# Kernel optimization log

Measured on AMD Instinct MI355X. Metric: run time of the kernel, lower is better.

## Reference

```python
import jax, jax.numpy as jnp
import numpy as np

T, K, D_SLOTS, D_IN, D_HID, EPSILON = 3, 11, 64, 128, 256, 1e-8


def _layer_norm(x, g, b, eps=1e-5):
    m = jnp.mean(x, axis=-1, keepdims=True)
    v = jnp.mean((x - m) ** 2, axis=-1, keepdims=True)
    return (x - m) * jax.lax.rsqrt(v + eps) * g + b


def _gru_cell(x, h, w_ih, w_hh, b_ih, b_hh):
    # torch.nn.GRUCell math; w_ih/w_hh stored as [D, 3D] (input-major)
    gx = x @ w_ih + b_ih
    gh = h @ w_hh + b_hh
    xr, xz, xn = jnp.split(gx, 3, axis=-1)
    hr, hz, hn = jnp.split(gh, 3, axis=-1)
    r = jax.nn.sigmoid(xr + hr)
    z = jax.nn.sigmoid(xz + hz)
    n = jnp.tanh(xn + r * hn)
    return (1.0 - z) * n + z * h


def setup_inputs() -> dict:
    key = jax.random.key(0)
    ks = jax.random.split(key, 12)
    B, N = 64, 4096
    s = 0.02
    return {
        "inputs": jax.random.normal(ks[0], (B, N, D_IN), jnp.float32),
        "ln_in_g": jnp.ones((D_IN,), jnp.float32),
        "ln_in_b": jnp.zeros((D_IN,), jnp.float32),
        "Wk": jax.random.normal(ks[1], (D_IN, D_SLOTS), jnp.float32) * s,
        "Wv": jax.random.normal(ks[2], (D_IN, D_SLOTS), jnp.float32) * s,
        "init_latents": jax.random.normal(ks[3], (1, K, D_SLOTS), jnp.float32),
        "ln_q_g": jnp.ones((D_SLOTS,), jnp.float32),
        "ln_q_b": jnp.zeros((D_SLOTS,), jnp.float32),
        "Wq": jax.random.normal(ks[4], (D_SLOTS, D_SLOTS), jnp.float32) * s,
        "w_ih": jax.random.normal(ks[5], (D_SLOTS, 3 * D_SLOTS), jnp.float32) * s,
        "w_hh": jax.random.normal(ks[6], (D_SLOTS, 3 * D_SLOTS), jnp.float32) * s,
        "b_ih": jnp.zeros((3 * D_SLOTS,), jnp.float32),
        "b_hh": jnp.zeros((3 * D_SLOTS,), jnp.float32),
        "ln_f_g": jnp.ones((D_SLOTS,), jnp.float32),
        "ln_f_b": jnp.zeros((D_SLOTS,), jnp.float32),
        "W1": jax.random.normal(ks[7], (D_SLOTS, D_HID), jnp.float32) * s,
        "b1": jnp.zeros((D_HID,), jnp.float32),
        "W2": jax.random.normal(ks[8], (D_HID, D_SLOTS), jnp.float32) * s,
        "b2": jnp.zeros((D_SLOTS,), jnp.float32),
    }


def reference(inputs, ln_in_g, ln_in_b, Wk, Wv, init_latents, ln_q_g, ln_q_b, Wq,
              w_ih, w_hh, b_ih, b_hh, ln_f_g, ln_f_b, W1, b1, W2, b2):
    B = inputs.shape[0]
    x = _layer_norm(inputs, ln_in_g, ln_in_b)          # [B,N,128]
    keys = x @ Wk                                       # [B,N,D]
    vals = x @ Wv                                       # [B,N,D]
    slots = jnp.broadcast_to(init_latents, (B, K, D_SLOTS))
    scale = D_SLOTS ** (-0.5)
    attn2 = None
    for _ in range(T):
        slots_prev = slots
        q = _layer_norm(slots, ln_q_g, ln_q_b) @ Wq     # [B,K,D]
        logits = scale * jnp.einsum('bnc,bmc->bnm', keys, q)  # [B,N,K]
        attn = jax.nn.softmax(logits, axis=-1) + EPSILON
        attn2 = attn
        attn_n = attn / jnp.sum(attn, axis=1, keepdims=True)   # competing norm over inputs
        updates = jnp.einsum('bnm,bnc->bmc', attn_n, vals)     # [B,K,D]
        slots = _gru_cell(updates.reshape(B * K, D_SLOTS),
                          slots_prev.reshape(B * K, D_SLOTS),
                          w_ih, w_hh, b_ih, b_hh).reshape(B, K, D_SLOTS)
        h = jax.nn.relu(_layer_norm(slots, ln_f_g, ln_f_b) @ W1 + b1)
        slots = slots + (h @ W2 + b2)
    return slots, attn2
```

## Files before the change

### kernel.cpp

```cpp
#include <hip/hip_runtime.h>

#define DIN   128
#define DSL   64
#define KSL   11
#define NTOK  4096
#define NB    64
#define NSPLIT 32
#define LN_EPS   1e-5f
#define ATTN_EPS 1e-8f
#define SCALE    0.125f

typedef __bf16 bf16x8 __attribute__((ext_vector_type(8)));
typedef float  f32x4  __attribute__((ext_vector_type(4)));

__global__ void k_prep(const float* __restrict__ Wk, const float* __restrict__ Wv,
                       const float* __restrict__ g, const float* __restrict__ b,
                       __bf16* __restrict__ WTf, float* __restrict__ EP) {
  if (blockIdx.x == 8) {
    const int c = threadIdx.x;
    if (c < 128) {
      const float* __restrict__ W = (c < 64) ? Wk : Wv;
      const int cc = c & 63;
      float G = 0.f, Bt = 0.f;
      for (int k = 0; k < 128; ++k) {
        const float w = W[k * 64 + cc];
        G += g[k] * w; Bt += b[k] * w;
      }
      EP[c] = G; EP[128 + c] = Bt;
    }
    return;
  }
  const int t = blockIdx.x * 256 + threadIdx.x;
  const int fid = t >> 6, lane = t & 63;
  const int ks = fid >> 3, nt = fid & 7;
  const int col = nt * 16 + (lane & 15);
  const int kb  = ks * 32 + (lane >> 4) * 8;
  union { uint4 u; __bf16 h[8]; } o;
#pragma unroll
  for (int j = 0; j < 8; ++j) {
    const int k = kb + j;
    const float v = ((col < 64) ? Wk[k * 64 + col] : Wv[k * 64 + (col - 64)]) * g[k];
    o.h[j] = (__bf16)v;
  }
  *((uint4*)WTf + t) = o.u;
}

__launch_bounds__(256)
__global__ void k_lnproj(const float* __restrict__ inp, const __bf16* __restrict__ WTf,
                         const float* __restrict__ EP, __bf16* __restrict__ keys,
                         __bf16* __restrict__ valsT) {
  __shared__ __bf16 Xs[4][16][136];
  __shared__ float rowstats[4][16][2];
  const int tid = threadIdx.x, wave = tid >> 6, lane = tid & 63;
  const int half = lane >> 5, hl = lane & 31;
  const int t = lane & 15, g = lane >> 4;
  const int rbase = blockIdx.x * 64 + wave * 16;

  float4 xr[8];
#pragma unroll
  for (int p = 0; p < 8; ++p)
    xr[p] = *(const float4*)(inp + (size_t)(rbase + 2 * p + half) * DIN + hl * 4);

  float s[8], sq[8];
#pragma unroll
  for (int p = 0; p < 8; ++p) {
    s[p]  = xr[p].x + xr[p].y + xr[p].z + xr[p].w;
    sq[p] = xr[p].x * xr[p].x + xr[p].y * xr[p].y + xr[p].z * xr[p].z + xr[p].w * xr[p].w;
    union { ushort4 u; __bf16 h[4]; } pk;
    pk.h[0] = (__bf16)xr[p].x; pk.h[1] = (__bf16)xr[p].y;
    pk.h[2] = (__bf16)xr[p].z; pk.h[3] = (__bf16)xr[p].w;
    *(ushort4*)&Xs[wave][2 * p + half][hl * 4] = pk.u;
  }

#pragma unroll
  for (int o = 16; o > 0; o >>= 1) {
#pragma unroll
    for (int p = 0; p < 8; ++p) { s[p] += __shfl_xor(s[p], o); sq[p] += __shfl_xor(sq[p], o); }
  }
  if (hl < 8) {
    const int p = hl;
    const float m = s[p] * (1.f / 128.f);
    const float rstd = rsqrtf(sq[p] * (1.f / 128.f) - m * m + LN_EPS);
    rowstats[wave][2 * p + half][0] = m;
    rowstats[wave][2 * p + half][1] = rstd;
  }

  const bf16x8* __restrict__ Wv8 = (const bf16x8*)WTf;
  bf16x8 wf[8];
#pragma unroll
  for (int nt = 0; nt < 8; ++nt) wf[nt] = Wv8[nt * 64 + lane];
  f32x4 acc[8] = {};
#pragma unroll
  for (int ks = 0; ks < 4; ++ks) {
    const bf16x8 xf = *(const bf16x8*)&Xs[wave][t][ks * 32 + g * 8];
    bf16x8 wn[8];
    if (ks < 3) {
#pragma unroll
      for (int nt = 0; nt < 8; ++nt) wn[nt] = Wv8[((ks + 1) * 8 + nt) * 64 + lane];
    }
#pragma unroll
    for (int nt = 0; nt < 8; ++nt)
      acc[nt] = __builtin_amdgcn_mfma_f32_16x16x32_bf16(wf[nt], xf, acc[nt], 0, 0, 0);
#pragma unroll
    for (int nt = 0; nt < 8; ++nt) wf[nt] = wn[nt];
  }

  const float2 mrs = *(const float2*)&rowstats[wave][t][0];
  const float rstd = mrs.y, mm = mrs.x * mrs.y;
  const int bidx = rbase >> 12;
  const int tIB  = (rbase & 4095) + t;
#pragma unroll
  for (int nt = 0; nt < 8; ++nt) {
    const float4 Gv = *(const float4*)(EP + nt * 16 + g * 4);
    const float4 Bv = *(const float4*)(EP + 128 + nt * 16 + g * 4);
    float o0 = rstd * acc[nt][0] - mm * Gv.x + Bv.x;
    float o1 = rstd * acc[nt][1] - mm * Gv.y + Bv.y;
    float o2 = rstd * acc[nt][2] - mm * Gv.z + Bv.z;
    float o3 = rstd * acc[nt][3] - mm * Gv.w + Bv.w;
    if (nt < 4) {
      union { unsigned long long u; __bf16 h[4]; } pk;
      pk.h[0] = (__bf16)o0; pk.h[1] = (__bf16)o1; pk.h[2] = (__bf16)o2; pk.h[3] = (__bf16)o3;
      *(unsigned long long*)&keys[(size_t)(rbase + t) * 64 + nt * 16 + g * 4] = pk.u;
    } else {
      const int vc = (nt - 4) * 16 + g * 4;
      valsT[((size_t)bidx * 64 + vc + 0) * NTOK + tIB] = (__bf16)o0;
      valsT[((size_t)bidx * 64 + vc + 1) * NTOK + tIB] = (__bf16)o1;
      valsT[((size_t)bidx * 64 + vc + 2) * NTOK + tIB] = (__bf16)o2;
      valsT[((size_t)bidx * 64 + vc + 3) * NTOK + tIB] = (__bf16)o3;
    }
  }
}

__global__ void k_init(const float* __restrict__ init_lat, const float* __restrict__ qg,
                       const float* __restrict__ qb, const float* __restrict__ Wq,
                       float* __restrict__ slots, float* __restrict__ q) {
  const int b = blockIdx.x;
  const int k = threadIdx.x >> 6, c = threadIdx.x & 63;
  const float s = init_lat[k * DSL + c];
  slots[(size_t)(b * KSL + k) * DSL + c] = s;
  float sum = s, sq = s * s;
#pragma unroll
  for (int o = 32; o > 0; o >>= 1) { sum += __shfl_xor(sum, o); sq += __shfl_xor(sq, o); }
  const float m = sum * (1.f / 64.f);
  const float rstd = rsqrtf(sq * (1.f / 64.f) - m * m + LN_EPS);
  const float qn = (s - m) * rstd * qg[c] + qb[c];
  float acc = 0.f;
  for (int i = 0; i < DSL; ++i) acc += __shfl(qn, i) * Wq[i * DSL + c];
  q[(size_t)(b * KSL + k) * DSL + c] = acc * SCALE;
}

__launch_bounds__(64)
__global__ void k_attn(const __bf16* __restrict__ keys, const __bf16* __restrict__ valsT,
                       const float* __restrict__ q, float* __restrict__ Upart,
                       float* __restrict__ Spart, float* __restrict__ attn_out) {
  __shared__ __bf16 P[2][16][72];
  const int b = blockIdx.x >> 5, sp = blockIdx.x & 31;
  const int lane = threadIdx.x;
  const int g = lane >> 4, t = lane & 15;

  bf16x8 qf[2];
#pragma unroll
  for (int ks = 0; ks < 2; ++ks) {
    float4 q0 = {0.f, 0.f, 0.f, 0.f}, q1 = {0.f, 0.f, 0.f, 0.f};
    if (t < KSL) {
      const float* __restrict__ qp = q + (size_t)(b * KSL + t) * DSL + ks * 32 + g * 8;
      q0 = *(const float4*)qp; q1 = *(const float4*)(qp + 4);
    }
    qf[ks][0] = (__bf16)q0.x; qf[ks][1] = (__bf16)q0.y;
    qf[ks][2] = (__bf16)q0.z; qf[ks][3] = (__bf16)q0.w;
    qf[ks][4] = (__bf16)q1.x; qf[ks][5] = (__bf16)q1.y;
    qf[ks][6] = (__bf16)q1.z; qf[ks][7] = (__bf16)q1.w;
  }

  const __bf16* __restrict__ kbase = keys + ((size_t)b * NTOK + sp * 128) * DSL;
  float sacc[4] = {0.f, 0.f, 0.f, 0.f};
  f32x4 U[4] = {};

#pragma unroll
  for (int gr = 0; gr < 2; ++gr) {
    const int tb = gr * 64;
#pragma unroll
    for (int tile = 0; tile < 4; ++tile) {
      f32x4 c = {};
#pragma unroll
      for (int ks = 0; ks < 2; ++ks) {
        const bf16x8 kf = *(const bf16x8*)(kbase + (size_t)(tb + tile * 16 + t) * DSL
                                           + ks * 32 + g * 8);
        c = __builtin_amdgcn_mfma_f32_16x16x32_bf16(qf[ks], kf, c, 0, 0, 0);
      }
      float lg[4];
#pragma unroll
      for (int r = 0; r < 4; ++r)
        lg[r] = (4 * g + r < KSL) ? c[r] : -1e30f;
      float mx = fmaxf(fmaxf(lg[0], lg[1]), fmaxf(lg[2], lg[3]));
      mx = fmaxf(mx, __shfl_xor(mx, 16));
      mx = fmaxf(mx, __shfl_xor(mx, 32));
      float e[4];
#pragma unroll
      for (int r = 0; r < 4; ++r) e[r] = __expf(lg[r] - mx);
      float se = e[0] + e[1] + e[2] + e[3];
      se += __shfl_xor(se, 16);
      se += __shfl_xor(se, 32);
      const float inv = 1.f / se;
#pragma unroll
      for (int r = 0; r < 4; ++r) {
        const float a = e[r] * inv + ATTN_EPS;
        sacc[r] += a;
        P[gr][4 * g + r][tile * 16 + t] = (__bf16)a;
        if (attn_out && 4 * g + r < KSL)
          attn_out[((size_t)b * NTOK + sp * 128 + tb + tile * 16 + t) * KSL + 4 * g + r] = a;
      }
    }
#pragma unroll
    for (int ks = 0; ks < 2; ++ks) {
      const bf16x8 pf = *(const bf16x8*)&P[gr][t][ks * 32 + g * 8];
#pragma unroll
      for (int ct = 0; ct < 4; ++ct) {
        const bf16x8 vf = *(const bf16x8*)(valsT + ((size_t)b * DSL + ct * 16 + t) * NTOK
                                           + sp * 128 + tb + ks * 32 + g * 8);
        U[ct] = __builtin_amdgcn_mfma_f32_16x16x32_bf16(pf, vf, U[ct], 0, 0, 0);
      }
    }
  }

  float* __restrict__ up = Upart + (size_t)(b * NSPLIT + sp) * (KSL * DSL);
#pragma unroll
  for (int ct = 0; ct < 4; ++ct)
#pragma unroll
    for (int r = 0; r < 4; ++r)
      if (4 * g + r < KSL) up[(4 * g + r) * DSL + ct * 16 + t] = U[ct][r];

#pragma unroll
  for (int r = 0; r < 4; ++r) {
#pragma unroll
    for (int o = 1; o < 16; o <<= 1) sacc[r] += __shfl_xor(sacc[r], o);
  }
  if (t == 0) {
    float* __restrict__ spp = Spart + (size_t)(b * NSPLIT + sp) * 16;
#pragma unroll
    for (int r = 0; r < 4; ++r) spp[4 * g + r] = sacc[r];
  }
}

__launch_bounds__(64)
__global__ void k_update(const float* __restrict__ Upart, const float* __restrict__ Spart,
                         float* __restrict__ slots, const float* __restrict__ w_ih,
                         const float* __restrict__ w_hh, const float* __restrict__ b_ih,
                         const float* __restrict__ b_hh, const float* __restrict__ fg,
                         const float* __restrict__ fb, const float* __restrict__ W1,
                         const float* __restrict__ b1v, const float* __restrict__ W2,
                         const float* __restrict__ b2v, const float* __restrict__ qg,
                         const float* __restrict__ qbv, const float* __restrict__ Wq,
                         float* __restrict__ q, float* __restrict__ out_slots) {
  const int row = blockIdx.x;
  const int c = threadIdx.x;
  const int b = row / 11, k = row - b * 11;

  float u = 0.f;
  for (int s = 0; s < NSPLIT; ++s)
    u += Upart[((size_t)(b * NSPLIT + s) * KSL + k) * DSL + c];
  float ss = 0.f;
  for (int s = 0; s < NSPLIT; ++s)
    ss += Spart[(size_t)(b * NSPLIT + s) * 16 + k];
  u /= ss;

  const float h = slots[(size_t)row * DSL + c];

  float gr = b_ih[c], gz = b_ih[64 + c], gn = b_ih[128 + c];
  float hr = b_hh[c], hz = b_hh[64 + c], hn = b_hh[128 + c];
  for (int i = 0; i < 64; ++i) {
    const float ui = __shfl(u, i), hi = __shfl(h, i);
    gr += ui * w_ih[i * 192 + c];       hr += hi * w_hh[i * 192 + c];
    gz += ui * w_ih[i * 192 + 64 + c];  hz += hi * w_hh[i * 192 + 64 + c];
    gn += ui * w_ih[i * 192 + 128 + c]; hn += hi * w_hh[i * 192 + 128 + c];
  }
  const float r = 1.f / (1.f + __expf(-(gr + hr)));
  const float z = 1.f / (1.f + __expf(-(gz + hz)));
  const float nn = tanhf(gn + r * hn);
  float sv = (1.f - z) * nn + z * h;

  float sum = sv, sq = sv * sv;
#pragma unroll
  for (int o = 32; o > 0; o >>= 1) { sum += __shfl_xor(sum, o); sq += __shfl_xor(sq, o); }
  float m = sum * (1.f / 64.f);
  float rstd = rsqrtf(sq * (1.f / 64.f) - m * m + LN_EPS);
  const float sl = (sv - m) * rstd * fg[c] + fb[c];

  float h0 = b1v[c], h1 = b1v[64 + c], h2 = b1v[128 + c], h3 = b1v[192 + c];
  for (int i = 0; i < 64; ++i) {
    const float si = __shfl(sl, i);
    h0 += si * W1[i * 256 + c];        h1 += si * W1[i * 256 + 64 + c];
    h2 += si * W1[i * 256 + 128 + c];  h3 += si * W1[i * 256 + 192 + c];
  }
  h0 = fmaxf(h0, 0.f); h1 = fmaxf(h1, 0.f); h2 = fmaxf(h2, 0.f); h3 = fmaxf(h3, 0.f);

  float o = b2v[c];
  for (int j = 0; j < 64; ++j) o += __shfl(h0, j) * W2[j * DSL + c];
  for (int j = 0; j < 64; ++j) o += __shfl(h1, j) * W2[(64 + j) * DSL + c];
  for (int j = 0; j < 64; ++j) o += __shfl(h2, j) * W2[(128 + j) * DSL + c];
  for (int j = 0; j < 64; ++j) o += __shfl(h3, j) * W2[(192 + j) * DSL + c];
  sv += o;

  slots[(size_t)row * DSL + c] = sv;
  if (out_slots) out_slots[(size_t)row * DSL + c] = sv;

  float s2 = sv, q2 = sv * sv;
#pragma unroll
  for (int o2 = 32; o2 > 0; o2 >>= 1) { s2 += __shfl_xor(s2, o2); q2 += __shfl_xor(q2, o2); }
  m = s2 * (1.f / 64.f);
  rstd = rsqrtf(q2 * (1.f / 64.f) - m * m + LN_EPS);
  const float qn = (sv - m) * rstd * qg[c] + qbv[c];
  float qa = 0.f;
  for (int i = 0; i < 64; ++i) qa += __shfl(qn, i) * Wq[i * DSL + c];
  q[(size_t)row * DSL + c] = qa * SCALE;
}

extern "C" void kernel_launch(void* const* d_in, const int* in_sizes, int n_in,
                              void* d_out, int out_size, void* d_ws, size_t ws_size,
                              hipStream_t stream) {
  const float* inp  = (const float*)d_in[0];
  const float* lng  = (const float*)d_in[1];
  const float* lnb  = (const float*)d_in[2];
  const float* Wk   = (const float*)d_in[3];
  const float* Wv   = (const float*)d_in[4];
  const float* init = (const float*)d_in[5];
  const float* qg   = (const float*)d_in[6];
  const float* qbb  = (const float*)d_in[7];
  const float* Wq   = (const float*)d_in[8];
  const float* wih  = (const float*)d_in[9];
  const float* whh  = (const float*)d_in[10];
  const float* bih  = (const float*)d_in[11];
  const float* bhh  = (const float*)d_in[12];
  const float* fg   = (const float*)d_in[13];
  const float* fb   = (const float*)d_in[14];
  const float* W1   = (const float*)d_in[15];
  const float* b1   = (const float*)d_in[16];
  const float* W2   = (const float*)d_in[17];
  const float* b2   = (const float*)d_in[18];

  char* wsb = (char*)d_ws;
  __bf16* keys  = (__bf16*)wsb;
  __bf16* valsT = keys + (size_t)NB * NTOK * DSL;
  __bf16* WTf   = valsT + (size_t)NB * DSL * NTOK;
  float* EP    = (float*)(WTf + 16384);
  float* slots = EP + 256;
  float* q     = slots + NB * KSL * DSL;
  float* Upart = q + NB * KSL * DSL;
  float* Spart = Upart + (size_t)NB * NSPLIT * KSL * DSL;

  float* out_slots = (float*)d_out;
  float* out_attn  = (float*)d_out + NB * KSL * DSL;

  k_prep<<<9, 256, 0, stream>>>(Wk, Wv, lng, lnb, WTf, EP);
  k_lnproj<<<4096, 256, 0, stream>>>(inp, WTf, EP, keys, valsT);
  k_init<<<NB, KSL * 64, 0, stream>>>(init, qg, qbb, Wq, slots, q);
  for (int t = 0; t < 3; ++t) {
    k_attn<<<NB * NSPLIT, 64, 0, stream>>>(keys, valsT, q, Upart, Spart,
                                           t == 2 ? out_attn : nullptr);
    k_update<<<NB * KSL, 64, 0, stream>>>(Upart, Spart, slots, wih, whh, bih, bhh,
                                          fg, fb, W1, b1, W2, b2, qg, qbb, Wq, q,
                                          t == 2 ? out_slots : nullptr);
  }
}
```

Baseline: 185.2 us.

## Split LN/projection into stats and proj kernels with LDS-transposed value stores

Splits the fused layernorm+projection kernel into a stats kernel that writes bf16 inputs and per-row mean/rstd to global memory, and a projection kernel that processes 32 tokens per wave with MFMA. The value outputs are staged through shared memory and written as coalesced 16-byte rows, replacing the scattered 2-byte transposed stores. The cost is an extra global round trip of the bf16 input copy plus an additional kernel launch.

```diff
diff --git a/kernel.cpp b/kernel.cpp
--- a/kernel.cpp
+++ b/kernel.cpp
@@ -46,14 +46,10 @@
 }
 
 __launch_bounds__(256)
-__global__ void k_lnproj(const float* __restrict__ inp, const __bf16* __restrict__ WTf,
-                         const float* __restrict__ EP, __bf16* __restrict__ keys,
-                         __bf16* __restrict__ valsT) {
-  __shared__ __bf16 Xs[4][16][136];
-  __shared__ float rowstats[4][16][2];
+__global__ void k_stats(const float* __restrict__ inp, __bf16* __restrict__ xbf,
+                        float2* __restrict__ stats) {
   const int tid = threadIdx.x, wave = tid >> 6, lane = tid & 63;
   const int half = lane >> 5, hl = lane & 31;
-  const int t = lane & 15, g = lane >> 4;
   const int rbase = blockIdx.x * 64 + wave * 16;
 
   float4 xr[8];
@@ -69,9 +65,8 @@
     union { ushort4 u; __bf16 h[4]; } pk;
     pk.h[0] = (__bf16)xr[p].x; pk.h[1] = (__bf16)xr[p].y;
     pk.h[2] = (__bf16)xr[p].z; pk.h[3] = (__bf16)xr[p].w;
-    *(ushort4*)&Xs[wave][2 * p + half][hl * 4] = pk.u;
-  }
-
+    *(ushort4*)&xbf[(size_t)(rbase + 2 * p + half) * DIN + hl * 4] = pk.u;
+  }
 #pragma unroll
   for (int o = 16; o > 0; o >>= 1) {
 #pragma unroll
@@ -81,54 +76,66 @@
     const int p = hl;
     const float m = s[p] * (1.f / 128.f);
     const float rstd = rsqrtf(sq[p] * (1.f / 128.f) - m * m + LN_EPS);
-    rowstats[wave][2 * p + half][0] = m;
-    rowstats[wave][2 * p + half][1] = rstd;
-  }
-
+    stats[rbase + 2 * p + half] = make_float2(m, rstd);
+  }
+}
+
+__launch_bounds__(256)
+__global__ void k_proj(const __bf16* __restrict__ xbf, const float2* __restrict__ stats,
+                       const __bf16* __restrict__ WTf, const float* __restrict__ EP,
+                       __bf16* __restrict__ keys, __bf16* __restrict__ valsT) {
+  __shared__ __bf16 VT[64][130];
+  const int tid = threadIdx.x, wave = tid >> 6, lane = tid & 63;
+  const int t = lane & 15, g = lane >> 4;
+  const int blkTok = blockIdx.x * 128;
+  const int tokbase = blkTok + wave * 32;
   const bf16x8* __restrict__ Wv8 = (const bf16x8*)WTf;
-  bf16x8 wf[8];
-#pragma unroll
-  for (int nt = 0; nt < 8; ++nt) wf[nt] = Wv8[nt * 64 + lane];
-  f32x4 acc[8] = {};
+
+  f32x4 acc[2][8] = {};
 #pragma unroll
   for (int ks = 0; ks < 4; ++ks) {
-    const bf16x8 xf = *(const bf16x8*)&Xs[wave][t][ks * 32 + g * 8];
-    bf16x8 wn[8];
-    if (ks < 3) {
-#pragma unroll
-      for (int nt = 0; nt < 8; ++nt) wn[nt] = Wv8[((ks + 1) * 8 + nt) * 64 + lane];
-    }
-#pragma unroll
-    for (int nt = 0; nt < 8; ++nt)
-      acc[nt] = __builtin_amdgcn_mfma_f32_16x16x32_bf16(wf[nt], xf, acc[nt], 0, 0, 0);
-#pragma unroll
-    for (int nt = 0; nt < 8; ++nt) wf[nt] = wn[nt];
-  }
-
-  const float2 mrs = *(const float2*)&rowstats[wave][t][0];
-  const float rstd = mrs.y, mm = mrs.x * mrs.y;
-  const int bidx = rbase >> 12;
-  const int tIB  = (rbase & 4095) + t;
-#pragma unroll
-  for (int nt = 0; nt < 8; ++nt) {
-    const float4 Gv = *(const float4*)(EP + nt * 16 + g * 4);
-    const float4 Bv = *(const float4*)(EP + 128 + nt * 16 + g * 4);
-    float o0 = rstd * acc[nt][0] - mm * Gv.x + Bv.x;
-    float o1 = rstd * acc[nt][1] - mm * Gv.y + Bv.y;
-    float o2 = rstd * acc[nt][2] - mm * Gv.z + Bv.z;
-    float o3 = rstd * acc[nt][3] - mm * Gv.w + Bv.w;
-    if (nt < 4) {
-      union { unsigned long long u; __bf16 h[4]; } pk;
-      pk.h[0] = (__bf16)o0; pk.h[1] = (__bf16)o1; pk.h[2] = (__bf16)o2; pk.h[3] = (__bf16)o3;
-      *(unsigned long long*)&keys[(size_t)(rbase + t) * 64 + nt * 16 + g * 4] = pk.u;
-    } else {
-      const int vc = (nt - 4) * 16 + g * 4;
-      valsT[((size_t)bidx * 64 + vc + 0) * NTOK + tIB] = (__bf16)o0;
-      valsT[((size_t)bidx * 64 + vc + 1) * NTOK + tIB] = (__bf16)o1;
-      valsT[((size_t)bidx * 64 + vc + 2) * NTOK + tIB] = (__bf16)o2;
-      valsT[((size_t)bidx * 64 + vc + 3) * NTOK + tIB] = (__bf16)o3;
-    }
-  }
+    const bf16x8 xf0 = *(const bf16x8*)&xbf[(size_t)(tokbase + t) * DIN + ks * 32 + g * 8];
+    const bf16x8 xf1 = *(const bf16x8*)&xbf[(size_t)(tokbase + 16 + t) * DIN + ks * 32 + g * 8];
+#pragma unroll
+    for (int nt = 0; nt < 8; ++nt) {
+      const bf16x8 wf = Wv8[(ks * 8 + nt) * 64 + lane];
+      acc[0][nt] = __builtin_amdgcn_mfma_f32_16x16x32_bf16(wf, xf0, acc[0][nt], 0, 0, 0);
+      acc[1][nt] = __builtin_amdgcn_mfma_f32_16x16x32_bf16(wf, xf1, acc[1][nt], 0, 0, 0);
+    }
+  }
+#pragma unroll
+  for (int tt = 0; tt < 2; ++tt) {
+    const float2 st = stats[tokbase + tt * 16 + t];
+    const float rstd = st.y, mm = st.x * st.y;
+#pragma unroll
+    for (int nt = 0; nt < 8; ++nt) {
+      const float4 Gv = *(const float4*)(EP + nt * 16 + g * 4);
+      const float4 Bv = *(const float4*)(EP + 128 + nt * 16 + g * 4);
+      const float o0 = rstd * acc[tt][nt][0] - mm * Gv.x + Bv.x;
+      const float o1 = rstd * acc[tt][nt][1] - mm * Gv.y + Bv.y;
+      const float o2 = rstd * acc[tt][nt][2] - mm * Gv.z + Bv.z;
+      const float o3 = rstd * acc[tt][nt][3] - mm * Gv.w + Bv.w;
+      if (nt < 4) {
+        union { unsigned long long u; __bf16 h[4]; } pk;
+        pk.h[0] = (__bf16)o0; pk.h[1] = (__bf16)o1; pk.h[2] = (__bf16)o2; pk.h[3] = (__bf16)o3;
+        *(unsigned long long*)&keys[(size_t)(tokbase + tt * 16 + t) * 64 + nt * 16 + g * 4] = pk.u;
+      } else {
+        const int ch = (nt - 4) * 16 + g * 4;
+        const int tk = wave * 32 + tt * 16 + t;
+        VT[ch + 0][tk] = (__bf16)o0;
+        VT[ch + 1][tk] = (__bf16)o1;
+        VT[ch + 2][tk] = (__bf16)o2;
+        VT[ch + 3][tk] = (__bf16)o3;
+      }
+    }
+  }
+  __syncthreads();
+  const int ch = tid >> 2, q = tid & 3;
+  const int bidx = blkTok >> 12, tIB = blkTok & 4095;
+  __bf16* __restrict__ vrow = valsT + ((size_t)bidx * 64 + ch) * NTOK + tIB;
+#pragma unroll
+  for (int s = 0; s < 4; ++s)
+    *(uint4*)&vrow[s * 32 + q * 8] = *(const uint4*)&VT[ch][s * 32 + q * 8];
 }
 
 __global__ void k_init(const float* __restrict__ init_lat, const float* __restrict__ qg,
@@ -341,9 +348,11 @@
   char* wsb = (char*)d_ws;
   __bf16* keys  = (__bf16*)wsb;
   __bf16* valsT = keys + (size_t)NB * NTOK * DSL;
-  __bf16* WTf   = valsT + (size_t)NB * DSL * NTOK;
-  float* EP    = (float*)(WTf + 16384);
-  float* slots = EP + 256;
+  __bf16* xbf   = valsT + (size_t)NB * DSL * NTOK;
+  __bf16* WTf   = xbf + (size_t)NB * NTOK * DIN;
+  float*  EP    = (float*)(WTf + 16384);
+  float2* stats = (float2*)(EP + 256);
+  float* slots = (float*)(stats + (size_t)NB * NTOK);
   float* q     = slots + NB * KSL * DSL;
   float* Upart = q + NB * KSL * DSL;
   float* Spart = Upart + (size_t)NB * NSPLIT * KSL * DSL;
@@ -352,7 +361,8 @@
   float* out_attn  = (float*)d_out + NB * KSL * DSL;
 
   k_prep<<<9, 256, 0, stream>>>(Wk, Wv, lng, lnb, WTf, EP);
-  k_lnproj<<<4096, 256, 0, stream>>>(inp, WTf, EP, keys, valsT);
+  k_stats<<<4096, 256, 0, stream>>>(inp, xbf, stats);
+  k_proj<<<2048, 256, 0, stream>>>(xbf, stats, WTf, EP, keys, valsT);
   k_init<<<NB, KSL * 64, 0, stream>>>(init, qg, qbb, Wq, slots, q);
   for (int t = 0; t < 3; ++t) {
     k_attn<<<NB * NSPLIT, 64, 0, stream>>>(keys, valsT, q, Upart, Spart,
```

Result: slower. 221.5 us (+19.6%).
